# Optimization experiments

Hardware: AMD Instinct MI355X
Metric: run time of the kernel (lower is better)

Reference implementation:

```python
import jax, jax.numpy as jnp
import numpy as np

MAXGRAD = 2.0
B, H, W, C = 8, 512, 512, 16


def _integral_image(x):
    # x: [B,H,W,2]; cumsum x-channel along width, y-channel along height
    x_s = jnp.cumsum(x[..., 0], axis=2)
    y_s = jnp.cumsum(x[..., 1], axis=1)
    return jnp.stack([x_s, y_s], axis=-1) - 1.0


def _normalize(grid):
    # grid: [B,H,W,2] -> rescale each row/col extent to [0, W-1] x [0, H-1]
    Hh, Ww = grid.shape[1], grid.shape[2]
    max_x = grid[:, :, -1:, 0]  # [B,H,1]
    min_x = grid[:, :, :1, 0]
    max_y = grid[:, -1:, :, 1]  # [B,1,W]
    min_y = grid[:, :1, :, 1]
    norm_x = (grid[..., 0] - min_x) / (max_x - min_x)
    norm_y = (grid[..., 1] - min_y) / (max_y - min_y)
    return jnp.stack([(Ww - 1) * norm_x, (Hh - 1) * norm_y], axis=-1)


def _resample2d(im, grid):
    # im: [B,H,W,C], grid: [B,H,W,2] in pixel coords; bilinear with border clamp
    Bb, Hh, Ww, _ = im.shape
    x = grid[..., 0]
    y = grid[..., 1]
    x0 = jnp.floor(x).astype(jnp.int32)
    x1 = x0 + 1
    y0 = jnp.floor(y).astype(jnp.int32)
    y1 = y0 + 1
    x0 = jnp.clip(x0, 0, Ww - 1)
    x1 = jnp.clip(x1, 0, Ww - 1)
    y0 = jnp.clip(y0, 0, Hh - 1)
    y1 = jnp.clip(y1, 0, Hh - 1)
    b = jnp.arange(Bb)[:, None, None]
    Ia = im[b, y0, x0]  # [B,H,W,C]
    Ib = im[b, y1, x0]
    Ic = im[b, y0, x1]
    Id = im[b, y1, x1]
    x0f = x0.astype(x.dtype)
    x1f = x1.astype(x.dtype)
    y0f = y0.astype(y.dtype)
    y1f = y1.astype(y.dtype)
    wa = ((x1f - x) * (y1f - y))[..., None]
    wb = ((x1f - x) * (y - y0f))[..., None]
    wc = ((x - x0f) * (y1f - y))[..., None]
    wd = ((x - x0f) * (y - y0f))[..., None]
    return wa * Ia + wb * Ib + wc * Ic + wd * Id


def setup_inputs() -> dict:
    key = jax.random.key(0)
    k1, k2, k3 = jax.random.split(key, 3)
    mov = jax.random.normal(k1, (B, H, W, C), dtype=jnp.float32)
    ref = jax.random.normal(k2, (B, H, W, C), dtype=jnp.float32)
    defgrad = jax.random.normal(k3, (B, H, W, 2), dtype=jnp.float32) * 0.1
    return {"mov": mov, "ref": ref, "defgrad": defgrad}


def reference(mov, ref, defgrad):
    c = MAXGRAD
    dg = c / (1.0 + (c - 1.0) * jnp.exp(-defgrad))  # logistic growth
    base_grid = _integral_image(jnp.ones_like(dg))
    sampling_grid = _integral_image(dg)
    grid_norm = _normalize(sampling_grid)
    grid_inv = 2.0 * base_grid - grid_norm
    mov_def = _resample2d(mov, grid_norm)
    ref_def = _resample2d(mov_def, grid_inv)
    return (mov_def, ref_def, grid_norm, grid_inv)
```

## Files before the change

### kernel.cpp

```cpp
#include <hip/hip_runtime.h>

#define Bn 8
#define Hn 512
#define Wn 512
#define Cn 16

typedef float fx4 __attribute__((ext_vector_type(4)));

__device__ __forceinline__ float dgf(float g) { return 2.0f / (1.0f + __expf(-g)); }

__global__ __launch_bounds__(512) void grid_kernel(const float* __restrict__ defgrad,
                                                   float* __restrict__ grid_norm,
                                                   float* __restrict__ grid_inv) {
    const int wave = threadIdx.x >> 6;
    const int lane = threadIdx.x & 63;

    if (blockIdx.x < 64) {
        __shared__ float partial[8][64];
        const int b  = blockIdx.x >> 3;
        const int w0 = (blockIdx.x & 7) * 64;
        const int w  = w0 + lane;
        const long cbase = ((long)b * Hn) * Wn + w;

        float e0 = dgf(defgrad[cbase * 2 + 1]);
        float sum = 0.f;
        #pragma unroll 8
        for (int i = 0; i < 64; ++i) {
            int h = (wave << 6) + i;
            sum += dgf(defgrad[(cbase + (long)h * Wn) * 2 + 1]);
        }
        partial[wave][lane] = sum;
        __syncthreads();
        float off = 0.f, tot = 0.f;
        #pragma unroll
        for (int j = 0; j < 8; ++j) {
            float p = partial[j][lane];
            if (j < wave) off += p;
            tot += p;
        }
        float denom = tot - e0;
        float run = off;
        #pragma unroll 8
        for (int i = 0; i < 64; ++i) {
            int h = (wave << 6) + i;
            long pidx = cbase + (long)h * Wn;
            run += dgf(defgrad[pidx * 2 + 1]);
            float norm = (h == Hn - 1) ? 511.0f : 511.0f * ((run - e0) / denom);
            grid_norm[pidx * 2 + 1] = norm;
            grid_inv[pidx * 2 + 1]  = 2.0f * (float)h - norm;
        }
    } else {
        __shared__ float wsum[8];
        __shared__ float s0sh;
        const int row = blockIdx.x - 64;
        const int t   = threadIdx.x;
        const long base = (long)row * Wn;

        float v = dgf(defgrad[(base + t) * 2]);
        float x = v;
        #pragma unroll
        for (int o = 1; o < 64; o <<= 1) {
            float n = __shfl_up(x, o, 64);
            x += (lane >= o) ? n : 0.0f;
        }
        if (lane == 63) wsum[wave] = x;
        if (t == 0)     s0sh = v;
        __syncthreads();
        float pre = 0.f, tot = 0.f;
        #pragma unroll
        for (int j = 0; j < 8; ++j) {
            float p = wsum[j];
            if (j < wave) pre += p;
            tot += p;
        }
        float scan = x + pre;
        float s0   = s0sh;
        float norm = (t == Wn - 1) ? 511.0f : 511.0f * ((scan - s0) / (tot - s0));
        long o = (base + t) * 2;
        grid_norm[o] = norm;
        grid_inv[o]  = 2.0f * (float)t - norm;
    }
}

__global__ __launch_bounds__(256) void resample_kernel(const float* __restrict__ im,
                                                       const float* __restrict__ grid,
                                                       float* __restrict__ out) {
    const int pix = blockIdx.x * 256 + threadIdx.x;
    const int bi  = pix >> 18;

    float2 g = *(const float2*)&grid[(long)pix * 2];
    float x = g.x, y = g.y;
    int x0 = (int)floorf(x);
    int y0 = (int)floorf(y);
    int x1 = x0 + 1, y1 = y0 + 1;
    x0 = min(max(x0, 0), Wn - 1);
    x1 = min(max(x1, 0), Wn - 1);
    y0 = min(max(y0, 0), Hn - 1);
    y1 = min(max(y1, 0), Hn - 1);
    float x0f = (float)x0, x1f = (float)x1, y0f = (float)y0, y1f = (float)y1;
    float wa = (x1f - x) * (y1f - y);
    float wb = (x1f - x) * (y - y0f);
    float wc = (x - x0f) * (y1f - y);
    float wd = (x - x0f) * (y - y0f);

    const float* base = im + ((long)bi << 22);
    const fx4* A = (const fx4*)(base + (((long)(y0 << 9) + x0) << 4));
    const fx4* Bp= (const fx4*)(base + (((long)(y1 << 9) + x0) << 4));
    const fx4* Cp= (const fx4*)(base + (((long)(y0 << 9) + x1) << 4));
    const fx4* Dp= (const fx4*)(base + (((long)(y1 << 9) + x1) << 4));
    fx4* O = (fx4*)(out + ((long)pix << 4));

    #pragma unroll
    for (int c = 0; c < 4; ++c) {
        fx4 a = A[c], b = Bp[c], cc = Cp[c], d = Dp[c];
        fx4 r = wa * a + wb * b + wc * cc + wd * d;
        __builtin_nontemporal_store(r, &O[c]);
    }
}

extern "C" void kernel_launch(void* const* d_in, const int* in_sizes, int n_in,
                              void* d_out, int out_size, void* d_ws, size_t ws_size,
                              hipStream_t stream) {
    const float* mov     = (const float*)d_in[0];
    const float* defgrad = (const float*)d_in[2];
    float* out = (float*)d_out;

    const long N_img  = (long)Bn * Hn * Wn * Cn;
    const long N_grid = (long)Bn * Hn * Wn * 2;
    float* mov_def   = out;
    float* ref_def   = out + N_img;
    float* grid_norm = out + 2 * N_img;
    float* grid_inv  = out + 2 * N_img + N_grid;

    grid_kernel<<<dim3(64 + Bn * Hn), dim3(512), 0, stream>>>(defgrad, grid_norm, grid_inv);

    const int npix = Bn * Hn * Wn;
    resample_kernel<<<dim3(npix / 256), dim3(256), 0, stream>>>(mov, grid_norm, mov_def);
    resample_kernel<<<dim3(npix / 256), dim3(256), 0, stream>>>(mov_def, grid_inv, ref_def);
}
```

Measured before the change: 618.5 us.

## Split each pixel's channels across four lanes in resample kernel

The resample kernel now has four adjacent threads cooperate on one pixel, each handling a 16-byte channel group, and each thread processes two pixels 64 apart. Neighbouring lanes therefore read contiguous 64-byte corner rows, and stores become fully coalesced instead of each thread striding 64 bytes apart. The grid computation and floor/clamp work are repeated four times per pixel, and the grid count doubles to match.

```diff
diff --git a/kernel.cpp b/kernel.cpp
--- a/kernel.cpp
+++ b/kernel.cpp
@@ -85,37 +85,48 @@
 __global__ __launch_bounds__(256) void resample_kernel(const float* __restrict__ im,
                                                        const float* __restrict__ grid,
                                                        float* __restrict__ out) {
-    const int pix = blockIdx.x * 256 + threadIdx.x;
-    const int bi  = pix >> 18;
+    const int tid = threadIdx.x;
+    const int cg  = tid & 3;
+    const int q   = tid >> 2;
+    const long p0 = (long)blockIdx.x * 128 + q;
+    const long p1 = p0 + 64;
 
-    float2 g = *(const float2*)&grid[(long)pix * 2];
-    float x = g.x, y = g.y;
-    int x0 = (int)floorf(x);
-    int y0 = (int)floorf(y);
-    int x1 = x0 + 1, y1 = y0 + 1;
-    x0 = min(max(x0, 0), Wn - 1);
-    x1 = min(max(x1, 0), Wn - 1);
-    y0 = min(max(y0, 0), Hn - 1);
-    y1 = min(max(y1, 0), Hn - 1);
-    float x0f = (float)x0, x1f = (float)x1, y0f = (float)y0, y1f = (float)y1;
-    float wa = (x1f - x) * (y1f - y);
-    float wb = (x1f - x) * (y - y0f);
-    float wc = (x - x0f) * (y1f - y);
-    float wd = (x - x0f) * (y - y0f);
+    float2 g0 = *(const float2*)&grid[p0 * 2];
+    float2 g1 = *(const float2*)&grid[p1 * 2];
 
-    const float* base = im + ((long)bi << 22);
-    const fx4* A = (const fx4*)(base + (((long)(y0 << 9) + x0) << 4));
-    const fx4* Bp= (const fx4*)(base + (((long)(y1 << 9) + x0) << 4));
-    const fx4* Cp= (const fx4*)(base + (((long)(y0 << 9) + x1) << 4));
-    const fx4* Dp= (const fx4*)(base + (((long)(y1 << 9) + x1) << 4));
-    fx4* O = (fx4*)(out + ((long)pix << 4));
+    int x0a = (int)floorf(g0.x), y0a = (int)floorf(g0.y);
+    int x1a = min(max(x0a + 1, 0), Wn - 1), y1a = min(max(y0a + 1, 0), Hn - 1);
+    x0a = min(max(x0a, 0), Wn - 1);  y0a = min(max(y0a, 0), Hn - 1);
+    int x0b = (int)floorf(g1.x), y0b = (int)floorf(g1.y);
+    int x1b = min(max(x0b + 1, 0), Wn - 1), y1b = min(max(y0b + 1, 0), Hn - 1);
+    x0b = min(max(x0b, 0), Wn - 1);  y0b = min(max(y0b, 0), Hn - 1);
 
-    #pragma unroll
-    for (int c = 0; c < 4; ++c) {
-        fx4 a = A[c], b = Bp[c], cc = Cp[c], d = Dp[c];
-        fx4 r = wa * a + wb * b + wc * cc + wd * d;
-        __builtin_nontemporal_store(r, &O[c]);
-    }
+    const float* base0 = im + ((p0 >> 18) << 22) + cg * 4;
+    const float* base1 = im + ((p1 >> 18) << 22) + cg * 4;
+
+    fx4 A0 = *(const fx4*)(base0 + (((long)(y0a << 9) + x0a) << 4));
+    fx4 B0 = *(const fx4*)(base0 + (((long)(y1a << 9) + x0a) << 4));
+    fx4 C0 = *(const fx4*)(base0 + (((long)(y0a << 9) + x1a) << 4));
+    fx4 D0 = *(const fx4*)(base0 + (((long)(y1a << 9) + x1a) << 4));
+    fx4 A1 = *(const fx4*)(base1 + (((long)(y0b << 9) + x0b) << 4));
+    fx4 B1 = *(const fx4*)(base1 + (((long)(y1b << 9) + x0b) << 4));
+    fx4 C1 = *(const fx4*)(base1 + (((long)(y0b << 9) + x1b) << 4));
+    fx4 D1 = *(const fx4*)(base1 + (((long)(y1b << 9) + x1b) << 4));
+
+    float wa0 = ((float)x1a - g0.x) * ((float)y1a - g0.y);
+    float wb0 = ((float)x1a - g0.x) * (g0.y - (float)y0a);
+    float wc0 = (g0.x - (float)x0a) * ((float)y1a - g0.y);
+    float wd0 = (g0.x - (float)x0a) * (g0.y - (float)y0a);
+    float wa1 = ((float)x1b - g1.x) * ((float)y1b - g1.y);
+    float wb1 = ((float)x1b - g1.x) * (g1.y - (float)y0b);
+    float wc1 = (g1.x - (float)x0b) * ((float)y1b - g1.y);
+    float wd1 = (g1.x - (float)x0b) * (g1.y - (float)y0b);
+
+    fx4 r0 = wa0 * A0 + wb0 * B0 + wc0 * C0 + wd0 * D0;
+    fx4 r1 = wa1 * A1 + wb1 * B1 + wc1 * C1 + wd1 * D1;
+
+    __builtin_nontemporal_store(r0, (fx4*)(out + (p0 << 4) + cg * 4));
+    __builtin_nontemporal_store(r1, (fx4*)(out + (p1 << 4) + cg * 4));
 }
 
 extern "C" void kernel_launch(void* const* d_in, const int* in_sizes, int n_in,
@@ -135,6 +146,6 @@
     grid_kernel<<<dim3(64 + Bn * Hn), dim3(512), 0, stream>>>(defgrad, grid_norm, grid_inv);
 
     const int npix = Bn * Hn * Wn;
-    resample_kernel<<<dim3(npix / 256), dim3(256), 0, stream>>>(mov, grid_norm, mov_def);
-    resample_kernel<<<dim3(npix / 256), dim3(256), 0, stream>>>(mov_def, grid_inv, ref_def);
+    resample_kernel<<<dim3(npix / 128), dim3(256), 0, stream>>>(mov, grid_norm, mov_def);
+    resample_kernel<<<dim3(npix / 128), dim3(256), 0, stream>>>(mov_def, grid_inv, ref_def);
 }
```

New measurement: 517.5 us. -16.3%, faster.
